# Optimization experiments

Measured on AMD Instinct MI355X. Metric: run time of the kernel, lower is better.

Reference implementation:

```python
import jax, jax.numpy as jnp
import numpy as np

N_HEADS = 16


def setup_inputs() -> dict:
    key = jax.random.key(0)
    k1, k2, k3 = jax.random.split(key, 3)
    B, T, C = 4, 2048, 1024
    x = jax.random.normal(k1, (B, T, C), dtype=jnp.float32)
    w_qkv = jax.random.normal(k2, (C, 3 * C), dtype=jnp.float32) * (C ** -0.5)
    w_proj = jax.random.normal(k3, (C, C), dtype=jnp.float32) * (C ** -0.5)
    return {"x": x, "w_qkv": w_qkv, "w_proj": w_proj}


def reference(x, w_qkv, w_proj):
    B, T, C = x.shape
    H = N_HEADS
    D = C // H
    qkv = x @ w_qkv  # [B,T,3C]
    q, k, v = jnp.split(qkv, 3, axis=2)
    # [B,T,C] -> [B,H,T,D]
    q = q.reshape(B, T, H, D).transpose(0, 2, 1, 3)
    k = k.reshape(B, T, H, D).transpose(0, 2, 1, 3)
    v = v.reshape(B, T, H, D).transpose(0, 2, 1, 3)
    att = jnp.einsum("bhqd,bhkd->bhqk", q, k) * (1.0 / D ** 0.5)
    causal = jnp.tril(jnp.ones((T, T), dtype=bool))
    att = jnp.where(causal[None, None], att, jnp.float32(-jnp.inf))
    att = jax.nn.softmax(att, axis=-1)
    y = jnp.einsum("bhqk,bhkd->bhqd", att, v)
    y = y.transpose(0, 2, 1, 3).reshape(B, T, C)
    return y @ w_proj
```

## Files before the change

kernel.cpp:

```cpp
#include <hip/hip_runtime.h>
#include <hip/hip_bf16.h>
#include <stdint.h>

using short8 = __attribute__((ext_vector_type(8))) short;
using s4vec  = __attribute__((ext_vector_type(4))) short;
using f32x4  = __attribute__((ext_vector_type(4))) float;

__device__ inline unsigned short f2bf(float f) {
  union { float f; unsigned int u; } v; v.f = f;
  unsigned int r = v.u + 0x7FFFu + ((v.u >> 16) & 1u);
  return (unsigned short)(r >> 16);
}
__device__ inline float bf2f(unsigned short u) {
  union { unsigned int u; float f; } v; v.u = ((unsigned int)u) << 16;
  return v.f;
}
__device__ inline unsigned int pack_bf16(float lo, float hi) {
  union { __hip_bfloat162 b; unsigned int u; } cv;
  cv.b = __float22bfloat162_rn(make_float2(lo, hi));
  return cv.u;
}

#if __has_builtin(__builtin_amdgcn_global_load_lds)
#define HAVE_GLOAD_LDS 1
__device__ inline void gload_lds16(const unsigned short* g, unsigned short* l) {
  auto gp = (const __attribute__((address_space(1))) unsigned int*)(uintptr_t)g;
  auto lp = (__attribute__((address_space(3))) unsigned int*)(uintptr_t)l;
  __builtin_amdgcn_global_load_lds(gp, lp, 16, 0, 0);
}
#else
#define HAVE_GLOAD_LDS 0
#endif

__global__ __launch_bounds__(256) void k_convert(const float* __restrict__ in,
                                                 unsigned short* __restrict__ out, int n) {
  int i = (blockIdx.x * 256 + threadIdx.x) * 8;
  if (i >= n) return;
  float4 a = *(const float4*)(in + i);
  float4 b = *(const float4*)(in + i + 4);
  short8 o;
  o[0] = (short)f2bf(a.x); o[1] = (short)f2bf(a.y);
  o[2] = (short)f2bf(a.z); o[3] = (short)f2bf(a.w);
  o[4] = (short)f2bf(b.x); o[5] = (short)f2bf(b.y);
  o[6] = (short)f2bf(b.z); o[7] = (short)f2bf(b.w);
  *(short8*)(out + i) = o;
}

__global__ __launch_bounds__(256) void k_transpose(const float* __restrict__ in,
                                                   unsigned short* __restrict__ out,
                                                   int R, int C) {
  __shared__ float t[32][33];
  int c0 = blockIdx.x * 32, r0 = blockIdx.y * 32;
  int cl = threadIdx.x & 31, rl = threadIdx.x >> 5;
  for (int p = 0; p < 4; ++p)
    t[rl + p * 8][cl] = in[(size_t)(r0 + rl + p * 8) * C + c0 + cl];
  __syncthreads();
  for (int p = 0; p < 4; ++p)
    out[(size_t)(c0 + rl + p * 8) * R + r0 + cl] = f2bf(t[cl][rl + p * 8]);
}

template <int MODE>
__global__ __launch_bounds__(256) void k_gemm(
    const unsigned short* __restrict__ A, const unsigned short* __restrict__ Bt,
    float* __restrict__ Cf,
    unsigned short* __restrict__ q_ws, unsigned short* __restrict__ k_ws,
    unsigned short* __restrict__ v_ws, int M, int N, int K) {
  __shared__ __align__(16) unsigned short As[128][32];
  __shared__ __align__(16) unsigned short Bs[128][32];
  const int tid = threadIdx.x;
  const int w = tid >> 6, l = tid & 63;
  const int lr = l & 15, lg = l >> 4;
  const int wr = w >> 1, wc = w & 1;
  const int m0 = blockIdx.y * 128, n0 = blockIdx.x * 128;
  f32x4 acc[4][4] = {};
  for (int k0 = 0; k0 < K; k0 += 32) {
#pragma unroll
    for (int rep = 0; rep < 2; ++rep) {
      int e = rep * 2048 + tid * 8;
      int row = e >> 5, kk = e & 31;
      const unsigned short* ga = A + (size_t)(m0 + row) * K + k0 + kk;
      const unsigned short* gb = Bt + (size_t)(n0 + row) * K + k0 + kk;
#if HAVE_GLOAD_LDS
      unsigned short* la = &As[0][0] + rep * 2048 + w * 512;
      unsigned short* lb = &Bs[0][0] + rep * 2048 + w * 512;
      gload_lds16(ga, la);
      gload_lds16(gb, lb);
#else
      *(short8*)&As[row][kk] = *(const short8*)ga;
      *(short8*)&Bs[row][kk] = *(const short8*)gb;
#endif
    }
    __syncthreads();
    short8 af[4], bf[4];
#pragma unroll
    for (int i = 0; i < 4; ++i) af[i] = *(const short8*)&As[wr * 64 + i * 16 + lr][lg * 8];
#pragma unroll
    for (int j = 0; j < 4; ++j) bf[j] = *(const short8*)&Bs[wc * 64 + j * 16 + lr][lg * 8];
#pragma unroll
    for (int i = 0; i < 4; ++i)
#pragma unroll
      for (int j = 0; j < 4; ++j)
        acc[i][j] = __builtin_amdgcn_mfma_f32_16x16x32_bf16(af[i], bf[j], acc[i][j], 0, 0, 0);
    __syncthreads();
  }
  if constexpr (MODE == 1) {
#pragma unroll
    for (int i = 0; i < 4; ++i)
#pragma unroll
      for (int j = 0; j < 4; ++j)
#pragma unroll
        for (int r = 0; r < 4; ++r) {
          int row = m0 + wr * 64 + i * 16 + lg * 4 + r;
          int col = n0 + wc * 64 + j * 16 + lr;
          Cf[(size_t)row * N + col] = acc[i][j][r];
        }
  } else {
#pragma unroll
    for (int i = 0; i < 4; ++i)
#pragma unroll
      for (int j = 0; j < 4; ++j) {
        int row0 = m0 + wr * 64 + i * 16 + lg * 4;
        int col = n0 + wc * 64 + j * 16 + lr;
        int b = row0 >> 11, t = row0 & 2047;
        int sect = col >> 10, c = col & 1023;
        int h = c >> 6, d = c & 63;
        if (sect == 2) {
          s4vec pv;
#pragma unroll
          for (int r = 0; r < 4; ++r) pv[r] = (short)f2bf(acc[i][j][r]);
          *(s4vec*)(v_ws + (((size_t)(b * 16 + h)) * 64 + d) * 2048 + t) = pv;
        } else {
          unsigned short* dst = (sect == 0) ? q_ws : k_ws;
#pragma unroll
          for (int r = 0; r < 4; ++r)
            dst[(((size_t)(b * 16 + h)) * 2048 + t + r) * 64 + d] = f2bf(acc[i][j][r]);
        }
      }
  }
}

__global__ __launch_bounds__(256) void k_attn(
    const unsigned short* __restrict__ q_ws, const unsigned short* __restrict__ k_ws,
    const unsigned short* __restrict__ vt_ws, unsigned short* __restrict__ y_ws) {
  __shared__ __align__(16) unsigned short Ks[64][72];
  __shared__ __align__(16) unsigned short Vs[64][72];
  const int bh = blockIdx.x;
  const int q0 = blockIdx.y * 128;
  const int tid = threadIdx.x, w = tid >> 6, l = tid & 63;
  const int lr = l & 15, lg = l >> 4;
  const unsigned short* Qp = q_ws + ((size_t)bh * 2048 + q0 + w * 32) * 64;
  const unsigned short* Kp = k_ws + (size_t)bh * 2048 * 64;
  const unsigned short* Vtp = vt_ws + (size_t)bh * 64 * 2048;
  short8 qf[2][2];
#pragma unroll
  for (int i = 0; i < 2; ++i)
#pragma unroll
    for (int ks = 0; ks < 2; ++ks) {
      short8 v = *(const short8*)(Qp + (i * 16 + lr) * 64 + ks * 32 + lg * 8);
#pragma unroll
      for (int e = 0; e < 8; ++e)
        v[e] = (short)f2bf(bf2f((unsigned short)v[e]) * 0.125f);
      qf[i][ks] = v;
    }
  float m_st[2] = {-INFINITY, -INFINITY}, l_st[2] = {0.f, 0.f};
  f32x4 o[2][4] = {};
  const int nt = (q0 >> 6) + 2;
  const int qhi = q0 + w * 32 + 31;
  const int srow = (tid * 8) >> 6, scc = (tid * 8) & 63;
  short8 kreg[2], vreg[2];
#pragma unroll
  for (int rep = 0; rep < 2; ++rep) {
    int row = srow + rep * 32;
    kreg[rep] = *(const short8*)(Kp + (size_t)row * 64 + scc);
    vreg[rep] = *(const short8*)(Vtp + (size_t)row * 2048 + scc);
  }
  for (int kt = 0; kt < nt; ++kt) {
    __syncthreads();
#pragma unroll
    for (int rep = 0; rep < 2; ++rep) {
      int row = srow + rep * 32;
      *(short8*)&Ks[row][scc] = kreg[rep];
      *(short8*)&Vs[row][scc] = vreg[rep];
    }
    __syncthreads();
    {
      int ktn = (kt + 1 < nt) ? kt + 1 : kt;
#pragma unroll
      for (int rep = 0; rep < 2; ++rep) {
        int row = srow + rep * 32;
        kreg[rep] = *(const short8*)(Kp + (size_t)(ktn * 64 + row) * 64 + scc);
        vreg[rep] = *(const short8*)(Vtp + (size_t)row * 2048 + ktn * 64 + scc);
      }
    }
    if (kt * 64 > qhi) continue;
    f32x4 s[4][2] = {};
#pragma unroll
    for (int ks = 0; ks < 2; ++ks) {
      short8 kf[4];
#pragma unroll
      for (int j = 0; j < 4; ++j) kf[j] = *(const short8*)&Ks[j * 16 + lr][ks * 32 + lg * 8];
#pragma unroll
      for (int j = 0; j < 4; ++j)
#pragma unroll
        for (int i = 0; i < 2; ++i)
          s[j][i] = __builtin_amdgcn_mfma_f32_16x16x32_bf16(kf[j], qf[i][ks], s[j][i], 0, 0, 0);
    }
    if (kt * 64 + 63 > q0 + w * 32) {
#pragma unroll
      for (int j = 0; j < 4; ++j)
#pragma unroll
        for (int i = 0; i < 2; ++i) {
          int gq = q0 + w * 32 + i * 16 + lr;
          int gk0 = kt * 64 + j * 16 + lg * 4;
#pragma unroll
          for (int r = 0; r < 4; ++r)
            if (gk0 + r > gq) s[j][i][r] = -INFINITY;
        }
    }
    union PaU { unsigned int u[4]; short8 v; };
    PaU pa[2][2];
#pragma unroll
    for (int i = 0; i < 2; ++i) {
      float tm = s[0][i][0];
#pragma unroll
      for (int j = 0; j < 4; ++j)
#pragma unroll
        for (int r = 0; r < 4; ++r) tm = fmaxf(tm, s[j][i][r]);
      tm = fmaxf(tm, __shfl_xor(tm, 16));
      tm = fmaxf(tm, __shfl_xor(tm, 32));
      if (!__all(tm <= m_st[i] + 8.f)) {
        float nm = fmaxf(m_st[i], tm);
        float corr = __expf(m_st[i] - nm);
        m_st[i] = nm;
        l_st[i] *= corr;
#pragma unroll
        for (int jd = 0; jd < 4; ++jd)
#pragma unroll
          for (int r = 0; r < 4; ++r) o[i][jd][r] *= corr;
      }
      float ts = 0.f;
#pragma unroll
      for (int j = 0; j < 4; ++j)
#pragma unroll
        for (int r = 0; r < 4; ++r) {
          float p = __expf(s[j][i][r] - m_st[i]);
          s[j][i][r] = p;
          ts += p;
        }
      ts += __shfl_xor(ts, 16);
      ts += __shfl_xor(ts, 32);
      l_st[i] += ts;
      unsigned int pk[4][2];
#pragma unroll
      for (int j = 0; j < 4; ++j)
#pragma unroll
        for (int h = 0; h < 2; ++h)
          pk[j][h] = pack_bf16(s[j][i][2 * h], s[j][i][2 * h + 1]);
#pragma unroll
      for (int ks = 0; ks < 2; ++ks)
#pragma unroll
        for (int wi = 0; wi < 4; ++wi) {
          int src = ((lg & 1) * 2 + (wi >> 1)) * 16 + lr;
          unsigned int w0 = __shfl(pk[ks * 2][wi & 1], src);
          unsigned int w1 = __shfl(pk[ks * 2 + 1][wi & 1], src);
          pa[i][ks].u[wi] = (lg >> 1) ? w1 : w0;
        }
    }
#pragma unroll
    for (int ks = 0; ks < 2; ++ks) {
      short8 vf[4];
#pragma unroll
      for (int jd = 0; jd < 4; ++jd) vf[jd] = *(const short8*)&Vs[jd * 16 + lr][ks * 32 + lg * 8];
#pragma unroll
      for (int i = 0; i < 2; ++i)
#pragma unroll
        for (int jd = 0; jd < 4; ++jd)
          o[i][jd] = __builtin_amdgcn_mfma_f32_16x16x32_bf16(vf[jd], pa[i][ks].v, o[i][jd], 0, 0, 0);
    }
  }
  int b = bh >> 4, h = bh & 15;
#pragma unroll
  for (int i = 0; i < 2; ++i) {
    float li = 1.f / l_st[i];
    int t = q0 + w * 32 + i * 16 + lr;
#pragma unroll
    for (int jd = 0; jd < 4; ++jd) {
      s4vec pv;
#pragma unroll
      for (int r = 0; r < 4; ++r) pv[r] = (short)f2bf(o[i][jd][r] * li);
      *(s4vec*)(y_ws + ((size_t)(b * 2048 + t)) * 1024 + h * 64 + jd * 16 + lg * 4) = pv;
    }
  }
}

extern "C" void kernel_launch(void* const* d_in, const int* in_sizes, int n_in,
                              void* d_out, int out_size, void* d_ws, size_t ws_size,
                              hipStream_t stream) {
  const float* x      = (const float*)d_in[0];
  const float* w_qkv  = (const float*)d_in[1];
  const float* w_proj = (const float*)d_in[2];
  float* out = (float*)d_out;
  const int Mm = 8192, Cc = 1024;
  unsigned short* ws     = (unsigned short*)d_ws;
  unsigned short* xb     = ws;
  unsigned short* wqkvT  = xb + (size_t)Mm * Cc;
  unsigned short* wprojT = wqkvT + (size_t)3 * Cc * Cc;
  unsigned short* q_ws   = wprojT + (size_t)Cc * Cc;
  unsigned short* k_ws   = q_ws + (size_t)Mm * Cc;
  unsigned short* vt_ws  = k_ws + (size_t)Mm * Cc;
  unsigned short* y_ws   = xb;

  k_convert<<<dim3(Mm * Cc / 8 / 256), 256, 0, stream>>>(x, xb, Mm * Cc);
  k_transpose<<<dim3(3 * Cc / 32, Cc / 32), 256, 0, stream>>>(w_qkv, wqkvT, Cc, 3 * Cc);
  k_transpose<<<dim3(Cc / 32, Cc / 32), 256, 0, stream>>>(w_proj, wprojT, Cc, Cc);
  k_gemm<0><<<dim3(3 * Cc / 128, Mm / 128), 256, 0, stream>>>(
      xb, wqkvT, nullptr, q_ws, k_ws, vt_ws, Mm, 3 * Cc, Cc);
  k_attn<<<dim3(64, 16), 256, 0, stream>>>(q_ws, k_ws, vt_ws, y_ws);
  k_gemm<1><<<dim3(Cc / 128, Mm / 128), 256, 0, stream>>>(
      y_ws, wprojT, out, nullptr, nullptr, nullptr, Mm, Cc, Cc);
}
```

Measured before the change: 306.6 us.

## XOR-swizzle K/V shared tiles and transpose P through per-wave LDS

Replaces the padded K/V shared-memory tiles with unpadded tiles whose 16-byte chunks are XOR-swizzled by row, so the fragment reads avoid bank conflicts without padding. It also stops using cross-lane shuffles to reshape the softmax probabilities into MFMA operand layout. Instead each wave writes packed bf16 probabilities to a swizzled per-wave LDS buffer and reads them back as 8-element fragments. This targets the many shuffle instructions and the bank conflicts, at the cost of extra LDS traffic and an LDS round trip within the wave.

```diff
diff --git a/kernel.cpp b/kernel.cpp
--- a/kernel.cpp
+++ b/kernel.cpp
@@ -5,6 +5,8 @@
 using short8 = __attribute__((ext_vector_type(8))) short;
 using s4vec  = __attribute__((ext_vector_type(4))) short;
 using f32x4  = __attribute__((ext_vector_type(4))) float;
+using u32x2  = __attribute__((ext_vector_type(2))) unsigned int;
+using u32x4  = __attribute__((ext_vector_type(4))) unsigned int;
 
 __device__ inline unsigned short f2bf(float f) {
   union { float f; unsigned int u; } v; v.f = f;
@@ -142,8 +144,9 @@
 __global__ __launch_bounds__(256) void k_attn(
     const unsigned short* __restrict__ q_ws, const unsigned short* __restrict__ k_ws,
     const unsigned short* __restrict__ vt_ws, unsigned short* __restrict__ y_ws) {
-  __shared__ __align__(16) unsigned short Ks[64][72];
-  __shared__ __align__(16) unsigned short Vs[64][72];
+  __shared__ __align__(16) unsigned short Ks[64][64];
+  __shared__ __align__(16) unsigned short Vs[64][64];
+  __shared__ __align__(16) unsigned int   Ps[4][32][32];
   const int bh = blockIdx.x;
   const int q0 = blockIdx.y * 128;
   const int tid = threadIdx.x, w = tid >> 6, l = tid & 63;
@@ -166,7 +169,11 @@
   f32x4 o[2][4] = {};
   const int nt = (q0 >> 6) + 2;
   const int qhi = q0 + w * 32 + 31;
-  const int srow = (tid * 8) >> 6, scc = (tid * 8) & 63;
+  const int srow = tid >> 3, cbl = tid & 7;
+  const int scc = cbl * 8;
+  const int scw = ((cbl ^ (srow & 7)) * 8);
+  const int fc0 = ((0 * 4 + lg) ^ (lr & 7)) * 8;
+  const int fc1 = ((1 * 4 + lg) ^ (lr & 7)) * 8;
   short8 kreg[2], vreg[2];
 #pragma unroll
   for (int rep = 0; rep < 2; ++rep) {
@@ -179,8 +186,8 @@
 #pragma unroll
     for (int rep = 0; rep < 2; ++rep) {
       int row = srow + rep * 32;
-      *(short8*)&Ks[row][scc] = kreg[rep];
-      *(short8*)&Vs[row][scc] = vreg[rep];
+      *(short8*)&Ks[row][scw] = kreg[rep];
+      *(short8*)&Vs[row][scw] = vreg[rep];
     }
     __syncthreads();
     {
@@ -196,9 +203,10 @@
     f32x4 s[4][2] = {};
 #pragma unroll
     for (int ks = 0; ks < 2; ++ks) {
+      int fc = ks ? fc1 : fc0;
       short8 kf[4];
 #pragma unroll
-      for (int j = 0; j < 4; ++j) kf[j] = *(const short8*)&Ks[j * 16 + lr][ks * 32 + lg * 8];
+      for (int j = 0; j < 4; ++j) kf[j] = *(const short8*)&Ks[j * 16 + lr][fc];
 #pragma unroll
       for (int j = 0; j < 4; ++j)
 #pragma unroll
@@ -217,8 +225,8 @@
             if (gk0 + r > gq) s[j][i][r] = -INFINITY;
         }
     }
-    union PaU { unsigned int u[4]; short8 v; };
-    PaU pa[2][2];
+    union U4S8 { u32x4 u; short8 s; };
+    short8 pa[2][2];
 #pragma unroll
     for (int i = 0; i < 2; ++i) {
       float tm = s[0][i][0];
@@ -250,32 +258,32 @@
       ts += __shfl_xor(ts, 16);
       ts += __shfl_xor(ts, 32);
       l_st[i] += ts;
-      unsigned int pk[4][2];
-#pragma unroll
-      for (int j = 0; j < 4; ++j)
-#pragma unroll
-        for (int h = 0; h < 2; ++h)
-          pk[j][h] = pack_bf16(s[j][i][2 * h], s[j][i][2 * h + 1]);
-#pragma unroll
-      for (int ks = 0; ks < 2; ++ks)
-#pragma unroll
-        for (int wi = 0; wi < 4; ++wi) {
-          int src = ((lg & 1) * 2 + (wi >> 1)) * 16 + lr;
-          unsigned int w0 = __shfl(pk[ks * 2][wi & 1], src);
-          unsigned int w1 = __shfl(pk[ks * 2 + 1][wi & 1], src);
-          pa[i][ks].u[wi] = (lg >> 1) ? w1 : w0;
-        }
+      unsigned int* prow = &Ps[w][i * 16 + lr][0];
+#pragma unroll
+      for (int j = 0; j < 4; ++j) {
+        u32x2 v2;
+        v2[0] = pack_bf16(s[j][i][0], s[j][i][1]);
+        v2[1] = pack_bf16(s[j][i][2], s[j][i][3]);
+        *(u32x2*)(prow + (((j * 4 + lg) ^ (lr & 14)) * 2)) = v2;
+      }
+#pragma unroll
+      for (int ks = 0; ks < 2; ++ks) {
+        U4S8 cv;
+        cv.u = *(const u32x4*)(prow + (((ks * 8 + lg * 2) ^ (lr & 14)) * 2));
+        pa[i][ks] = cv.s;
+      }
     }
 #pragma unroll
     for (int ks = 0; ks < 2; ++ks) {
+      int fc = ks ? fc1 : fc0;
       short8 vf[4];
 #pragma unroll
-      for (int jd = 0; jd < 4; ++jd) vf[jd] = *(const short8*)&Vs[jd * 16 + lr][ks * 32 + lg * 8];
+      for (int jd = 0; jd < 4; ++jd) vf[jd] = *(const short8*)&Vs[jd * 16 + lr][fc];
 #pragma unroll
       for (int i = 0; i < 2; ++i)
 #pragma unroll
         for (int jd = 0; jd < 4; ++jd)
-          o[i][jd] = __builtin_amdgcn_mfma_f32_16x16x32_bf16(vf[jd], pa[i][ks].v, o[i][jd], 0, 0, 0);
+          o[i][jd] = __builtin_amdgcn_mfma_f32_16x16x32_bf16(vf[jd], pa[i][ks], o[i][jd], 0, 0, 0);
     }
   }
   int b = bh >> 4, h = bh & 15;
```

Result: faster. 291.6 us (-4.9%).
